# Kernel tuning notes

Measured on AMD Instinct MI355X. Metric: run time of the kernel, lower is better.

## Reference

```python
import jax, jax.numpy as jnp
import numpy as np

N_HEAD = 16
ROPE_BASE = 10000.0


def _rope_cache(T, head_dim):
    # half-split RoPE: cos/sin of shape [T, head_dim//2]
    half = head_dim // 2
    inv_freq = ROPE_BASE ** (-jnp.arange(half, dtype=jnp.float32) / half)
    angles = jnp.arange(T, dtype=jnp.float32)[:, None] * inv_freq[None, :]  # [T, half]
    return jnp.cos(angles), jnp.sin(angles)


def _apply_rope(x, cos, sin):
    # x: [B, H, T, D]; cos/sin: [T, D//2]
    half = x.shape[-1] // 2
    x1, x2 = x[..., :half], x[..., half:]
    c = cos[None, None, :, :]
    s = sin[None, None, :, :]
    return jnp.concatenate([x1 * c - x2 * s, x1 * s + x2 * c], axis=-1)


def setup_inputs() -> dict:
    key = jax.random.key(0)
    k1, k2, k3 = jax.random.split(key, 3)
    B, T, C = 2, 2048, 1024
    x = jax.random.normal(k1, (B, T, C), dtype=jnp.float32)
    w_attn = jax.random.normal(k2, (C, 3 * C), dtype=jnp.float32) * (C ** -0.5)
    b_attn = jnp.zeros((3 * C,), dtype=jnp.float32)
    w_proj = jax.random.normal(k3, (C, C), dtype=jnp.float32) * (C ** -0.5)
    b_proj = jnp.zeros((C,), dtype=jnp.float32)
    return {"x": x, "w_attn": w_attn, "b_attn": b_attn, "w_proj": w_proj, "b_proj": b_proj}


def reference(x, w_attn, b_attn, w_proj, b_proj):
    B, T, C = x.shape
    H = N_HEAD
    hd = C // H

    qkv = x @ w_attn + b_attn                      # [B, T, 3C] fused QKV
    q, k, v = jnp.split(qkv, 3, axis=-1)
    q = q.reshape(B, T, H, hd).transpose(0, 2, 1, 3)  # [B, H, T, hd]
    k = k.reshape(B, T, H, hd).transpose(0, 2, 1, 3)
    v = v.reshape(B, T, H, hd).transpose(0, 2, 1, 3)

    cos, sin = _rope_cache(T, hd)
    q = _apply_rope(q, cos, sin)
    k = _apply_rope(k, cos, sin)

    scale = 1.0 / jnp.sqrt(jnp.float32(hd))
    att = jnp.einsum("bhqd,bhkd->bhqk", q, k) * scale  # [B, H, T, T]
    causal = jnp.tril(jnp.ones((T, T), dtype=bool))
    att = jnp.where(causal[None, None], att, -jnp.inf)
    att = jax.nn.softmax(att, axis=-1)
    y = jnp.einsum("bhqk,bhkd->bhqd", att, v)          # [B, H, T, hd]
    y = y.transpose(0, 2, 1, 3).reshape(B, T, C)
    return y @ w_proj + b_proj
```

## Files before the change

### kernel.cpp

```cpp
#include <hip/hip_runtime.h>
#include <hip/hip_bf16.h>
#include <cmath>

typedef _Float16 half_t;
typedef half_t half4 __attribute__((ext_vector_type(4)));
typedef half_t half8 __attribute__((ext_vector_type(8)));
typedef float f32x4 __attribute__((ext_vector_type(4)));

#define N_HEADS 16
#define HD      64
#define T_SEQ   2048
#define B_SZ    2
#define C_DIM   1024
#define M_ROWS  (B_SZ * T_SEQ)
#define N_QKV   (3 * C_DIM)
#define QSCALE  0.18033688f

__device__ inline void load_lds16(const half_t* g, half_t* l) {
  __builtin_amdgcn_global_load_lds(
      (const __attribute__((address_space(1))) void*)g,
      (__attribute__((address_space(3))) void*)l, 16, 0, 0);
}

__global__ __launch_bounds__(256) void k_prep(const float* __restrict__ x,
                                              half_t* __restrict__ xb,
                                              const float* __restrict__ wa,
                                              half_t* __restrict__ wT,
                                              const float* __restrict__ wp,
                                              half_t* __restrict__ wpT) {
  __shared__ float tile[64][65];
  int bid = blockIdx.x, tid = threadIdx.x;
  if (bid < 4096) {
    int i = (bid * 256 + tid) * 4;
    float4 v = *(const float4*)(x + i);
    half_t o[4] = {(half_t)v.x, (half_t)v.y, (half_t)v.z, (half_t)v.w};
    *(ulong1*)(xb + i) = *(ulong1*)o;
    return;
  }
  const float* in; half_t* out; int K, N, id;
  if (bid < 4096 + 768) { id = bid - 4096; in = wa; out = wT;  K = 1024; N = 3072; }
  else                  { id = bid - 4864; in = wp; out = wpT; K = 1024; N = 1024; }
  int n0 = (id % (N / 64)) * 64, k0 = (id / (N / 64)) * 64;
  int tx = tid & 63, ty = tid >> 6;
  #pragma unroll
  for (int i = 0; i < 64; i += 4)
    tile[ty + i][tx] = in[(size_t)(k0 + ty + i) * N + n0 + tx];
  __syncthreads();
  #pragma unroll
  for (int i = 0; i < 64; i += 4) {
    int r = ty + i;
    out[(size_t)(n0 + r) * K + k0 + tx] = (half_t)tile[tx][r];
  }
}

template <typename OT, int TN>
__global__ __launch_bounds__(256) void k_gemm(const half_t* __restrict__ A,
                                              const half_t* __restrict__ Bt,
                                              const float* __restrict__ bias,
                                              OT* __restrict__ C,
                                              int M, int N, int K) {
  constexpr int NI = TN / 32;
  __shared__ half_t As[128 * 64];
  __shared__ half_t Bs[TN * 64];
  int tid = threadIdx.x;
  int wave = tid >> 6, lane = tid & 63;
  int lane15 = lane & 15, quad = lane >> 4;
  int wm = (wave >> 1) * 64, wn = (wave & 1) * (TN / 2);
  int bm0 = blockIdx.y * 128, bn0 = blockIdx.x * TN;
  f32x4 acc[4][NI] = {};

  for (int kb = 0; kb < K; kb += 64) {
    const half_t* Ag = A + (size_t)bm0 * K + kb;
    const half_t* Bg = Bt + (size_t)bn0 * K + kb;
    __syncthreads();
    #pragma unroll
    for (int p = 0; p < 4; p++) {
      int fc = wave * 4 * 64 + p * 64 + lane;
      int r = fc >> 3, c = (fc & 7) ^ (r & 7);
      load_lds16(Ag + (size_t)r * K + c * 8, As + (wave * 4 + p) * 512);
    }
    #pragma unroll
    for (int p = 0; p < NI; p++) {
      int fc = wave * NI * 64 + p * 64 + lane;
      int r = fc >> 3, c = (fc & 7) ^ (r & 7);
      load_lds16(Bg + (size_t)r * K + c * 8, Bs + (wave * NI + p) * 512);
    }
    __syncthreads();
    #pragma unroll
    for (int ks = 0; ks < 2; ks++) {
      half8 af[4], bf[NI];
      #pragma unroll
      for (int i = 0; i < 4; i++) {
        int Ra = wm + i * 16 + lane15;
        af[i] = *(const half8*)(As + Ra * 64 + ((ks * 4 + quad) ^ (Ra & 7)) * 8);
      }
      #pragma unroll
      for (int i = 0; i < NI; i++) {
        int Rb = wn + i * 16 + lane15;
        bf[i] = *(const half8*)(Bs + Rb * 64 + ((ks * 4 + quad) ^ (Rb & 7)) * 8);
      }
      #pragma unroll
      for (int mi = 0; mi < 4; mi++)
        #pragma unroll
        for (int ni = 0; ni < NI; ni++)
          acc[mi][ni] = __builtin_amdgcn_mfma_f32_16x16x32_f16(af[mi], bf[ni], acc[mi][ni], 0, 0, 0);
    }
  }
  #pragma unroll
  for (int mi = 0; mi < 4; mi++)
    #pragma unroll
    for (int ni = 0; ni < NI; ni++) {
      int n = bn0 + wn + ni * 16 + lane15;
      float bv = bias[n];
      int mrow = bm0 + wm + mi * 16 + quad * 4;
      #pragma unroll
      for (int r = 0; r < 4; r++)
        C[(size_t)(mrow + r) * N + n] = (OT)(acc[mi][ni][r] + bv);
    }
}

__global__ __launch_bounds__(256) void k_rope(const half_t* __restrict__ qkv,
                                              half_t* __restrict__ Q,
                                              half_t* __restrict__ Ko,
                                              half_t* __restrict__ Vt) {
  __shared__ float vt[64][65];
  int bh = blockIdx.y;
  int b = bh >> 4, h = bh & 15;
  int t0 = blockIdx.x * 64;
  int tid = threadIdx.x;
  int trow = tid >> 5, i = tid & 31;
  float inv = exp2f(-(float)i * (13.287712379549449f / 32.0f));
  #pragma unroll
  for (int p = 0; p < 8; p++) {
    int tloc = p * 8 + trow;
    int t = t0 + tloc;
    const half_t* row = qkv + (size_t)(b * T_SEQ + t) * N_QKV;
    float q1 = (float)row[h * 64 + i],        q2 = (float)row[h * 64 + i + 32];
    float k1 = (float)row[1024 + h * 64 + i], k2 = (float)row[1024 + h * 64 + i + 32];
    float v1 = (float)row[2048 + h * 64 + i], v2 = (float)row[2048 + h * 64 + i + 32];
    float s, c;
    sincosf((float)t * inv, &s, &c);
    size_t base = ((size_t)bh * T_SEQ + t) * HD;
    Q[base + i]       = (half_t)((q1 * c - q2 * s) * QSCALE);
    Q[base + i + 32]  = (half_t)((q1 * s + q2 * c) * QSCALE);
    Ko[base + i]      = (half_t)(k1 * c - k2 * s);
    Ko[base + i + 32] = (half_t)(k1 * s + k2 * c);
    vt[i][tloc]      = v1;
    vt[i + 32][tloc] = v2;
  }
  __syncthreads();
  int d = tid >> 6, tc = tid & 63;
  #pragma unroll
  for (int p = 0; p < 16; p++) {
    int dd = p * 4 + d;
    Vt[((size_t)bh * HD + dd) * T_SEQ + t0 + tc] = (half_t)vt[dd][tc];
  }
}

__global__ __launch_bounds__(256) void k_flash(const half_t* __restrict__ Qg,
                                               const half_t* __restrict__ Kg,
                                               const half_t* __restrict__ Vg,
                                               half_t* __restrict__ y) {
  __shared__ half_t Ks[2][4096];
  __shared__ half_t Vs[2][4096];
  int bh = blockIdx.y;
  int b = bh >> 4, h = bh & 15;
  const int Cm[4] = {0, 31, 1, 30};
  int qt = (int)blockIdx.x ^ Cm[(blockIdx.y >> 3) & 3];
  int tid = threadIdx.x;
  int wave = tid >> 6, lane = tid & 63;
  int lane15 = lane & 15, quad = lane >> 4;
  const half_t* Qb = Qg + (size_t)bh * T_SEQ * HD;
  const half_t* Kb = Kg + (size_t)bh * T_SEQ * HD;
  const half_t* Vb = Vg + (size_t)bh * HD * T_SEQ;

  #define STAGE(buf, kv0)                                                      \
    {                                                                          \
      _Pragma("unroll")                                                        \
      for (int pp = 0; pp < 2; pp++) {                                         \
        int fc = (wave * 2 + pp) * 64 + lane;                                  \
        int rr = fc >> 3, cc = (fc & 7) ^ (rr & 7);                            \
        load_lds16(Kb + (size_t)((kv0) + rr) * HD + cc * 8,                    \
                   &Ks[buf][0] + fc * 8);                                      \
        load_lds16(Vb + (size_t)rr * T_SEQ + (kv0) + cc * 8,                   \
                   &Vs[buf][0] + fc * 8);                                      \
      }                                                                        \
    }

  int q0 = qt * 64;
  int qrow = q0 + wave * 16 + lane15;
  half8 bq0 = *(const half8*)(Qb + (size_t)qrow * HD + quad * 8);
  half8 bq1 = *(const half8*)(Qb + (size_t)qrow * HD + 32 + quad * 8);
  f32x4 ot[4] = {};
  float l = 0.f;

  STAGE(0, 0);
  for (int j = 0; j < qt; j++) {
    int buf = j & 1;
    __syncthreads();
    STAGE(buf ^ 1, (j + 1) * 64);
    const half_t* Kt = &Ks[buf][0];
    const half_t* Vt = &Vs[buf][0];
    f32x4 sacc[4];
    #pragma unroll
    for (int s = 0; s < 4; s++) {
      int R = s * 16 + lane15;
      half8 ak0 = *(const half8*)(Kt + R * 64 + ((quad) ^ (R & 7)) * 8);
      half8 ak1 = *(const half8*)(Kt + R * 64 + ((4 + quad) ^ (R & 7)) * 8);
      f32x4 z = {};
      z = __builtin_amdgcn_mfma_f32_16x16x32_f16(ak0, bq0, z, 0, 0, 0);
      sacc[s] = __builtin_amdgcn_mfma_f32_16x16x32_f16(ak1, bq1, z, 0, 0, 0);
    }
    #pragma unroll
    for (int s = 0; s < 4; s++) {
      half4 bp;
      #pragma unroll
      for (int r = 0; r < 4; r++) {
        float p = exp2f(fminf(sacc[s][r], 14.0f));
        l += p;
        bp[r] = (half_t)p;
      }
      #pragma unroll
      for (int nm = 0; nm < 4; nm++) {
        int Rv = nm * 16 + lane15;
        half4 av = *(const half4*)(Vt + Rv * 64 +
                                   ((2 * s + (quad >> 1)) ^ (Rv & 7)) * 8 +
                                   (quad & 1) * 4);
        ot[nm] = __builtin_amdgcn_mfma_f32_16x16x16f16(av, bp, ot[nm], 0, 0, 0);
      }
    }
  }
  {
    int buf = qt & 1;
    __syncthreads();
    const half_t* Kt = &Ks[buf][0];
    const half_t* Vt = &Vs[buf][0];
    f32x4 sacc[4];
    #pragma unroll
    for (int s = 0; s < 4; s++) {
      int R = s * 16 + lane15;
      half8 ak0 = *(const half8*)(Kt + R * 64 + ((quad) ^ (R & 7)) * 8);
      half8 ak1 = *(const half8*)(Kt + R * 64 + ((4 + quad) ^ (R & 7)) * 8);
      f32x4 z = {};
      z = __builtin_amdgcn_mfma_f32_16x16x32_f16(ak0, bq0, z, 0, 0, 0);
      sacc[s] = __builtin_amdgcn_mfma_f32_16x16x32_f16(ak1, bq1, z, 0, 0, 0);
    }
    #pragma unroll
    for (int s = 0; s < 4; s++) {
      half4 bp;
      #pragma unroll
      for (int r = 0; r < 4; r++) {
        float sv = sacc[s][r];
        if (s * 16 + quad * 4 + r > wave * 16 + lane15) sv = -1.0e30f;
        float p = exp2f(fminf(sv, 14.0f));
        l += p;
        bp[r] = (half_t)p;
      }
      #pragma unroll
      for (int nm = 0; nm < 4; nm++) {
        int Rv = nm * 16 + lane15;
        half4 av = *(const half4*)(Vt + Rv * 64 +
                                   ((2 * s + (quad >> 1)) ^ (Rv & 7)) * 8 +
                                   (quad & 1) * 4);
        ot[nm] = __builtin_amdgcn_mfma_f32_16x16x16f16(av, bp, ot[nm], 0, 0, 0);
      }
    }
  }

  l += __shfl_xor(l, 16);
  l += __shfl_xor(l, 32);
  float invl = 1.0f / l;
  int t = q0 + wave * 16 + lane15;
  half_t* yr = y + (size_t)(b * T_SEQ + t) * C_DIM + h * 64;
  #pragma unroll
  for (int nm = 0; nm < 4; nm++) {
    half4 o4;
    #pragma unroll
    for (int r = 0; r < 4; r++) o4[r] = (half_t)(ot[nm][r] * invl);
    *(half4*)(yr + nm * 16 + quad * 4) = o4;
  }
  #undef STAGE
}

extern "C" void kernel_launch(void* const* d_in, const int* in_sizes, int n_in,
                              void* d_out, int out_size, void* d_ws, size_t ws_size,
                              hipStream_t stream) {
  const float* x      = (const float*)d_in[0];
  const float* w_attn = (const float*)d_in[1];
  const float* b_attn = (const float*)d_in[2];
  const float* w_proj = (const float*)d_in[3];
  const float* b_proj = (const float*)d_in[4];
  float* out = (float*)d_out;

  char* ws = (char*)d_ws;
  const size_t MB = 1u << 20;
  half_t* xb  = (half_t*)(ws);
  half_t* wT  = (half_t*)(ws + 8 * MB);
  half_t* wpT = (half_t*)(ws + 14 * MB);
  half_t* Q   = (half_t*)(ws + 16 * MB);
  half_t* Kb  = (half_t*)(ws + 24 * MB);
  half_t* Vt  = (half_t*)(ws + 32 * MB);
  half_t* qkv = (half_t*)(ws + 40 * MB);
  half_t* y   = (half_t*)(ws + 40 * MB);

  k_prep<<<4096 + 768 + 256, 256, 0, stream>>>(x, xb, w_attn, wT, w_proj, wpT);
  k_gemm<half_t, 128><<<dim3(N_QKV / 128, M_ROWS / 128), 256, 0, stream>>>(
      xb, wT, b_attn, qkv, M_ROWS, N_QKV, C_DIM);
  k_rope<<<dim3(T_SEQ / 64, B_SZ * N_HEADS), 256, 0, stream>>>(qkv, Q, Kb, Vt);
  k_flash<<<dim3(32, B_SZ * N_HEADS), 256, 0, stream>>>(Q, Kb, Vt, y);
  k_gemm<float, 64><<<dim3(C_DIM / 64, M_ROWS / 128), 256, 0, stream>>>(
      y, wpT, b_proj, out, M_ROWS, C_DIM, C_DIM);
}
```

Baseline: 196.3 us.

## Enlarge flash-attention query tile to 128 rows with eight waves per block

```diff
diff --git a/kernel.cpp b/kernel.cpp
--- a/kernel.cpp
+++ b/kernel.cpp
@@ -157,7 +157,7 @@
   }
 }
 
-__global__ __launch_bounds__(256) void k_flash(const half_t* __restrict__ Qg,
+__global__ __launch_bounds__(512) void k_flash(const half_t* __restrict__ Qg,
                                                const half_t* __restrict__ Kg,
                                                const half_t* __restrict__ Vg,
                                                half_t* __restrict__ y) {
@@ -165,8 +165,7 @@
   __shared__ half_t Vs[2][4096];
   int bh = blockIdx.y;
   int b = bh >> 4, h = bh & 15;
-  const int Cm[4] = {0, 31, 1, 30};
-  int qt = (int)blockIdx.x ^ Cm[(blockIdx.y >> 3) & 3];
+  int qt = (bh < 16) ? (int)blockIdx.x : 15 - (int)blockIdx.x;
   int tid = threadIdx.x;
   int wave = tid >> 6, lane = tid & 63;
   int lane15 = lane & 15, quad = lane >> 4;
@@ -176,18 +175,15 @@
 
   #define STAGE(buf, kv0)                                                      \
     {                                                                          \
-      _Pragma("unroll")                                                        \
-      for (int pp = 0; pp < 2; pp++) {                                         \
-        int fc = (wave * 2 + pp) * 64 + lane;                                  \
-        int rr = fc >> 3, cc = (fc & 7) ^ (rr & 7);                            \
-        load_lds16(Kb + (size_t)((kv0) + rr) * HD + cc * 8,                    \
-                   &Ks[buf][0] + fc * 8);                                      \
-        load_lds16(Vb + (size_t)rr * T_SEQ + (kv0) + cc * 8,                   \
-                   &Vs[buf][0] + fc * 8);                                      \
-      }                                                                        \
-    }
-
-  int q0 = qt * 64;
+      int fc = wave * 64 + lane;                                               \
+      int rr = fc >> 3, cc = (fc & 7) ^ (rr & 7);                              \
+      load_lds16(Kb + (size_t)((kv0) + rr) * HD + cc * 8,                      \
+                 &Ks[buf][0] + fc * 8);                                        \
+      load_lds16(Vb + (size_t)rr * T_SEQ + (kv0) + cc * 8,                     \
+                 &Vs[buf][0] + fc * 8);                                        \
+    }
+
+  int q0 = qt * 128;
   int qrow = q0 + wave * 16 + lane15;
   half8 bq0 = *(const half8*)(Qb + (size_t)qrow * HD + quad * 8);
   half8 bq1 = *(const half8*)(Qb + (size_t)qrow * HD + 32 + quad * 8);
@@ -195,7 +191,7 @@
   float l = 0.f;
 
   STAGE(0, 0);
-  for (int j = 0; j < qt; j++) {
+  for (int j = 0; j < 2 * qt; j++) {
     int buf = j & 1;
     __syncthreads();
     STAGE(buf ^ 1, (j + 1) * 64);
@@ -231,8 +227,10 @@
     }
   }
   {
-    int buf = qt & 1;
-    __syncthreads();
+    int j = 2 * qt;
+    int buf = j & 1;
+    __syncthreads();
+    STAGE(buf ^ 1, (j + 1) * 64);
     const half_t* Kt = &Ks[buf][0];
     const half_t* Vt = &Vs[buf][0];
     f32x4 sacc[4];
@@ -263,6 +261,45 @@
                                    ((2 * s + (quad >> 1)) ^ (Rv & 7)) * 8 +
                                    (quad & 1) * 4);
         ot[nm] = __builtin_amdgcn_mfma_f32_16x16x16f16(av, bp, ot[nm], 0, 0, 0);
+      }
+    }
+  }
+  {
+    int j = 2 * qt + 1;
+    int buf = j & 1;
+    __syncthreads();
+    if (wave >= 4) {
+      const half_t* Kt = &Ks[buf][0];
+      const half_t* Vt = &Vs[buf][0];
+      f32x4 sacc[4];
+      #pragma unroll
+      for (int s = 0; s < 4; s++) {
+        int R = s * 16 + lane15;
+        half8 ak0 = *(const half8*)(Kt + R * 64 + ((quad) ^ (R & 7)) * 8);
+        half8 ak1 = *(const half8*)(Kt + R * 64 + ((4 + quad) ^ (R & 7)) * 8);
+        f32x4 z = {};
+        z = __builtin_amdgcn_mfma_f32_16x16x32_f16(ak0, bq0, z, 0, 0, 0);
+        sacc[s] = __builtin_amdgcn_mfma_f32_16x16x32_f16(ak1, bq1, z, 0, 0, 0);
+      }
+      #pragma unroll
+      for (int s = 0; s < 4; s++) {
+        half4 bp;
+        #pragma unroll
+        for (int r = 0; r < 4; r++) {
+          float sv = sacc[s][r];
+          if (s * 16 + quad * 4 + r > (wave - 4) * 16 + lane15) sv = -1.0e30f;
+          float p = exp2f(fminf(sv, 14.0f));
+          l += p;
+          bp[r] = (half_t)p;
+        }
+        #pragma unroll
+        for (int nm = 0; nm < 4; nm++) {
+          int Rv = nm * 16 + lane15;
+          half4 av = *(const half4*)(Vt + Rv * 64 +
+                                     ((2 * s + (quad >> 1)) ^ (Rv & 7)) * 8 +
+                                     (quad & 1) * 4);
+          ot[nm] = __builtin_amdgcn_mfma_f32_16x16x16f16(av, bp, ot[nm], 0, 0, 0);
+        }
       }
     }
   }
@@ -307,7 +344,7 @@
   k_gemm<half_t, 128><<<dim3(N_QKV / 128, M_ROWS / 128), 256, 0, stream>>>(
       xb, wT, b_attn, qkv, M_ROWS, N_QKV, C_DIM);
   k_rope<<<dim3(T_SEQ / 64, B_SZ * N_HEADS), 256, 0, stream>>>(qkv, Q, Kb, Vt);
-  k_flash<<<dim3(32, B_SZ * N_HEADS), 256, 0, stream>>>(Q, Kb, Vt, y);
+  k_flash<<<dim3(16, B_SZ * N_HEADS), 512, 0, stream>>>(Q, Kb, Vt, y);
   k_gemm<float, 64><<<dim3(C_DIM / 64, M_ROWS / 128), 256, 0, stream>>>(
       y, wpT, b_proj, out, M_ROWS, C_DIM, C_DIM);
 }
```

After: 201.4 us. 2.6% more time.

## Split KV tiles across two wave groups and pair causal query tiles per block

Applied to the files above, without the earlier changes.

```diff
diff --git a/kernel.cpp b/kernel.cpp
--- a/kernel.cpp
+++ b/kernel.cpp
@@ -157,129 +157,146 @@
   }
 }
 
-__global__ __launch_bounds__(256) void k_flash(const half_t* __restrict__ Qg,
+__device__ __forceinline__ void sched_noop() {}
+
+template <bool DIAG>
+__device__ __forceinline__ void tile_mfma(const half_t* __restrict__ Kt,
+                                          const half_t* __restrict__ Vt,
+                                          half8 bq0, half8 bq1,
+                                          f32x4 (&ot)[4], float& l,
+                                          int lane15, int quad, int qloc) {
+  f32x4 sacc[4];
+  #pragma unroll
+  for (int s = 0; s < 4; s++) {
+    int R_ = s * 16 + lane15;
+    half8 ak0 = *(const half8*)(Kt + R_ * 64 + ((quad) ^ (R_ & 7)) * 8);
+    half8 ak1 = *(const half8*)(Kt + R_ * 64 + ((4 + quad) ^ (R_ & 7)) * 8);
+    f32x4 z = {};
+    z = __builtin_amdgcn_mfma_f32_16x16x32_f16(ak0, bq0, z, 0, 0, 0);
+    sacc[s] = __builtin_amdgcn_mfma_f32_16x16x32_f16(ak1, bq1, z, 0, 0, 0);
+  }
+  #pragma unroll
+  for (int s = 0; s < 4; s++) {
+    half4 bp;
+    #pragma unroll
+    for (int r = 0; r < 4; r++) {
+      float sv = sacc[s][r];
+      if (DIAG && (s * 16 + quad * 4 + r > qloc)) sv = -1.0e30f;
+      float p = exp2f(fminf(sv, 14.0f));
+      l += p;
+      bp[r] = (half_t)p;
+    }
+    #pragma unroll
+    for (int nm = 0; nm < 4; nm++) {
+      int Rv = nm * 16 + lane15;
+      half4 av = *(const half4*)(Vt + Rv * 64 +
+                                 ((2 * s + (quad >> 1)) ^ (Rv & 7)) * 8 +
+                                 (quad & 1) * 4);
+      ot[nm] = __builtin_amdgcn_mfma_f32_16x16x16f16(av, bp, ot[nm], 0, 0, 0);
+    }
+  }
+}
+
+#define STAGE2(bb, j0, j1)                                                     \
+  {                                                                            \
+    int fc = wave * 64 + lane;                                                 \
+    int rr_ = fc >> 3, cc = (fc & 7) ^ (rr_ & 7);                              \
+    load_lds16(Kb + (size_t)((j0) * 64 + rr_) * HD + cc * 8,                   \
+               &Ks[bb][0][0] + fc * 8);                                        \
+    load_lds16(Kb + (size_t)((j1) * 64 + rr_) * HD + cc * 8,                   \
+               &Ks[bb][1][0] + fc * 8);                                        \
+    load_lds16(Vb + (size_t)rr_ * T_SEQ + (j0) * 64 + cc * 8,                  \
+               &Vs[bb][0][0] + fc * 8);                                        \
+    load_lds16(Vb + (size_t)rr_ * T_SEQ + (j1) * 64 + cc * 8,                  \
+               &Vs[bb][1][0] + fc * 8);                                        \
+  }
+
+__device__ __forceinline__ void process_tile(
+    int qt, const half_t* __restrict__ Qb, const half_t* __restrict__ Kb,
+    const half_t* __restrict__ Vb, half_t* __restrict__ y, int b, int h,
+    half_t (&Ks)[2][2][4096], half_t (&Vs)[2][2][4096],
+    int wave, int lane, int g, int wq, int lane15, int quad) {
+  int q0 = qt * 64;
+  int qrow = q0 + wq * 16 + lane15;
+  half8 bq0 = *(const half8*)(Qb + (size_t)qrow * HD + quad * 8);
+  half8 bq1 = *(const half8*)(Qb + (size_t)qrow * HD + 32 + quad * 8);
+  f32x4 ot[4] = {};
+  float l = 0.f;
+  int R = (qt + 2) >> 1;
+  for (int r = 0; r < R - 1; r++) {
+    __syncthreads();
+    int nj = 2 * (r + 1);
+    int nj1 = (nj + 1 <= qt) ? nj + 1 : qt;
+    STAGE2((r + 1) & 1, nj, nj1);
+    tile_mfma<false>(&Ks[r & 1][g][0], &Vs[r & 1][g][0], bq0, bq1, ot, l,
+                     lane15, quad, 0);
+  }
+  __syncthreads();
+  {
+    int jtl = 2 * (R - 1) + g;
+    const half_t* Kt = &Ks[(R - 1) & 1][g][0];
+    const half_t* Vt = &Vs[(R - 1) & 1][g][0];
+    if (jtl == qt)
+      tile_mfma<true>(Kt, Vt, bq0, bq1, ot, l, lane15, quad, wq * 16 + lane15);
+    else if (jtl < qt)
+      tile_mfma<false>(Kt, Vt, bq0, bq1, ot, l, lane15, quad, 0);
+  }
+  l += __shfl_xor(l, 16);
+  l += __shfl_xor(l, 32);
+  __syncthreads();
+  float* cb = (float*)&Ks[0][0][0];
+  int ci = (wq * 64 + lane) * 17;
+  if (g == 1) {
+    #pragma unroll
+    for (int nm = 0; nm < 4; nm++)
+      #pragma unroll
+      for (int r = 0; r < 4; r++) cb[ci + nm * 4 + r] = ot[nm][r];
+    cb[ci + 16] = l;
+  }
+  __syncthreads();
+  if (g == 0) {
+    #pragma unroll
+    for (int nm = 0; nm < 4; nm++)
+      #pragma unroll
+      for (int r = 0; r < 4; r++) ot[nm][r] += cb[ci + nm * 4 + r];
+    l += cb[ci + 16];
+    float invl = 1.0f / l;
+    int t = q0 + wq * 16 + lane15;
+    half_t* yr = y + (size_t)(b * T_SEQ + t) * C_DIM + h * 64;
+    #pragma unroll
+    for (int nm = 0; nm < 4; nm++) {
+      half4 o4;
+      #pragma unroll
+      for (int r = 0; r < 4; r++) o4[r] = (half_t)(ot[nm][r] * invl);
+      *(half4*)(yr + nm * 16 + quad * 4) = o4;
+    }
+  }
+  __syncthreads();
+}
+
+__global__ __launch_bounds__(512) void k_flash(const half_t* __restrict__ Qg,
                                                const half_t* __restrict__ Kg,
                                                const half_t* __restrict__ Vg,
                                                half_t* __restrict__ y) {
-  __shared__ half_t Ks[2][4096];
-  __shared__ half_t Vs[2][4096];
+  __shared__ half_t Ks[2][2][4096];
+  __shared__ half_t Vs[2][2][4096];
   int bh = blockIdx.y;
   int b = bh >> 4, h = bh & 15;
-  const int Cm[4] = {0, 31, 1, 30};
-  int qt = (int)blockIdx.x ^ Cm[(blockIdx.y >> 3) & 3];
+  int x = blockIdx.x;
   int tid = threadIdx.x;
   int wave = tid >> 6, lane = tid & 63;
+  int g = wave >> 2, wq = wave & 3;
   int lane15 = lane & 15, quad = lane >> 4;
   const half_t* Qb = Qg + (size_t)bh * T_SEQ * HD;
   const half_t* Kb = Kg + (size_t)bh * T_SEQ * HD;
   const half_t* Vb = Vg + (size_t)bh * HD * T_SEQ;
 
-  #define STAGE(buf, kv0)                                                      \
-    {                                                                          \
-      _Pragma("unroll")                                                        \
-      for (int pp = 0; pp < 2; pp++) {                                         \
-        int fc = (wave * 2 + pp) * 64 + lane;                                  \
-        int rr = fc >> 3, cc = (fc & 7) ^ (rr & 7);                            \
-        load_lds16(Kb + (size_t)((kv0) + rr) * HD + cc * 8,                    \
-                   &Ks[buf][0] + fc * 8);                                      \
-        load_lds16(Vb + (size_t)rr * T_SEQ + (kv0) + cc * 8,                   \
-                   &Vs[buf][0] + fc * 8);                                      \
-      }                                                                        \
-    }
-
-  int q0 = qt * 64;
-  int qrow = q0 + wave * 16 + lane15;
-  half8 bq0 = *(const half8*)(Qb + (size_t)qrow * HD + quad * 8);
-  half8 bq1 = *(const half8*)(Qb + (size_t)qrow * HD + 32 + quad * 8);
-  f32x4 ot[4] = {};
-  float l = 0.f;
-
-  STAGE(0, 0);
-  for (int j = 0; j < qt; j++) {
-    int buf = j & 1;
-    __syncthreads();
-    STAGE(buf ^ 1, (j + 1) * 64);
-    const half_t* Kt = &Ks[buf][0];
-    const half_t* Vt = &Vs[buf][0];
-    f32x4 sacc[4];
-    #pragma unroll
-    for (int s = 0; s < 4; s++) {
-      int R = s * 16 + lane15;
-      half8 ak0 = *(const half8*)(Kt + R * 64 + ((quad) ^ (R & 7)) * 8);
-      half8 ak1 = *(const half8*)(Kt + R * 64 + ((4 + quad) ^ (R & 7)) * 8);
-      f32x4 z = {};
-      z = __builtin_amdgcn_mfma_f32_16x16x32_f16(ak0, bq0, z, 0, 0, 0);
-      sacc[s] = __builtin_amdgcn_mfma_f32_16x16x32_f16(ak1, bq1, z, 0, 0, 0);
-    }
-    #pragma unroll
-    for (int s = 0; s < 4; s++) {
-      half4 bp;
-      #pragma unroll
-      for (int r = 0; r < 4; r++) {
-        float p = exp2f(fminf(sacc[s][r], 14.0f));
-        l += p;
-        bp[r] = (half_t)p;
-      }
-      #pragma unroll
-      for (int nm = 0; nm < 4; nm++) {
-        int Rv = nm * 16 + lane15;
-        half4 av = *(const half4*)(Vt + Rv * 64 +
-                                   ((2 * s + (quad >> 1)) ^ (Rv & 7)) * 8 +
-                                   (quad & 1) * 4);
-        ot[nm] = __builtin_amdgcn_mfma_f32_16x16x16f16(av, bp, ot[nm], 0, 0, 0);
-      }
-    }
-  }
-  {
-    int buf = qt & 1;
-    __syncthreads();
-    const half_t* Kt = &Ks[buf][0];
-    const half_t* Vt = &Vs[buf][0];
-    f32x4 sacc[4];
-    #pragma unroll
-    for (int s = 0; s < 4; s++) {
-      int R = s * 16 + lane15;
-      half8 ak0 = *(const half8*)(Kt + R * 64 + ((quad) ^ (R & 7)) * 8);
-      half8 ak1 = *(const half8*)(Kt + R * 64 + ((4 + quad) ^ (R & 7)) * 8);
-      f32x4 z = {};
-      z = __builtin_amdgcn_mfma_f32_16x16x32_f16(ak0, bq0, z, 0, 0, 0);
-      sacc[s] = __builtin_amdgcn_mfma_f32_16x16x32_f16(ak1, bq1, z, 0, 0, 0);
-    }
-    #pragma unroll
-    for (int s = 0; s < 4; s++) {
-      half4 bp;
-      #pragma unroll
-      for (int r = 0; r < 4; r++) {
-        float sv = sacc[s][r];
-        if (s * 16 + quad * 4 + r > wave * 16 + lane15) sv = -1.0e30f;
-        float p = exp2f(fminf(sv, 14.0f));
-        l += p;
-        bp[r] = (half_t)p;
-      }
-      #pragma unroll
-      for (int nm = 0; nm < 4; nm++) {
-        int Rv = nm * 16 + lane15;
-        half4 av = *(const half4*)(Vt + Rv * 64 +
-                                   ((2 * s + (quad >> 1)) ^ (Rv & 7)) * 8 +
-                                   (quad & 1) * 4);
-        ot[nm] = __builtin_amdgcn_mfma_f32_16x16x16f16(av, bp, ot[nm], 0, 0, 0);
-      }
-    }
-  }
-
-  l += __shfl_xor(l, 16);
-  l += __shfl_xor(l, 32);
-  float invl = 1.0f / l;
-  int t = q0 + wave * 16 + lane15;
-  half_t* yr = y + (size_t)(b * T_SEQ + t) * C_DIM + h * 64;
-  #pragma unroll
-  for (int nm = 0; nm < 4; nm++) {
-    half4 o4;
-    #pragma unroll
-    for (int r = 0; r < 4; r++) o4[r] = (half_t)(ot[nm][r] * invl);
-    *(half4*)(yr + nm * 16 + quad * 4) = o4;
-  }
-  #undef STAGE
+  int qtA = x, qtB = 31 - x;
+  STAGE2(0, 0, (qtA >= 1 ? 1 : 0));
+  process_tile(qtA, Qb, Kb, Vb, y, b, h, Ks, Vs, wave, lane, g, wq, lane15, quad);
+  STAGE2(0, 0, 1);
+  process_tile(qtB, Qb, Kb, Vb, y, b, h, Ks, Vs, wave, lane, g, wq, lane15, quad);
+  #undef STAGE2
 }
 
 extern "C" void kernel_launch(void* const* d_in, const int* in_sizes, int n_in,
@@ -307,7 +324,7 @@
   k_gemm<half_t, 128><<<dim3(N_QKV / 128, M_ROWS / 128), 256, 0, stream>>>(
       xb, wT, b_attn, qkv, M_ROWS, N_QKV, C_DIM);
   k_rope<<<dim3(T_SEQ / 64, B_SZ * N_HEADS), 256, 0, stream>>>(qkv, Q, Kb, Vt);
-  k_flash<<<dim3(32, B_SZ * N_HEADS), 256, 0, stream>>>(Q, Kb, Vt, y);
+  k_flash<<<dim3(16, B_SZ * N_HEADS), 512, 0, stream>>>(Q, Kb, Vt, y);
   k_gemm<float, 64><<<dim3(C_DIM / 64, M_ROWS / 128), 256, 0, stream>>>(
       y, wpT, b_proj, out, M_ROWS, C_DIM, C_DIM);
 }
```

Result: no change. 194.4 us (-1.0%).
